# Optimization experiments

Measured on AMD Instinct MI355X. Metric: run time of the kernel, lower is better.

The kernel has to match this reference:

```python
import jax, jax.numpy as jnp
import numpy as np

NUM_GRAPHS = 512
N_NODES = 500000
C = 256
R = 16

def setup_inputs() -> dict:
    key = jax.random.key(0)
    k1, k2, k3, k4 = jax.random.split(key, 4)
    x = jax.random.normal(k1, (N_NODES, C), dtype=jnp.float32)
    batch = jnp.sort(jax.random.randint(k2, (N_NODES,), 0, NUM_GRAPHS, dtype=jnp.int64))
    # Linear weights (torch stores [out,in]; we use [in,out] for x @ W)
    W1 = jax.random.normal(k3, (C, C // R), dtype=jnp.float32) * (1.0 / np.sqrt(C))
    W2 = jax.random.normal(k4, (C // R, C), dtype=jnp.float32) * (1.0 / np.sqrt(C // R))
    return {"x": x, "batch": batch, "W1": W1, "W2": W2}

def reference(x, batch, W1, W2):
    batch = batch.astype(jnp.int32)
    # segment mean pool: [G, C]
    seg_sum = jax.ops.segment_sum(x, batch, num_segments=NUM_GRAPHS)
    counts = jax.ops.segment_sum(jnp.ones((x.shape[0],), x.dtype), batch, num_segments=NUM_GRAPHS)
    mean_pool = seg_sum / jnp.maximum(counts, 1.0)[:, None]
    # squeeze-excite MLP: Linear -> ReLU -> Linear -> Sigmoid
    scale = jax.nn.sigmoid(jax.nn.relu(mean_pool @ W1) @ W2)  # [G, C]
    # repeat_interleave(scale, bincount(batch)) on sorted batch == gather by batch
    return x * scale[batch]
```

## Files before the change

### kernel.cpp

```cpp
#include <hip/hip_runtime.h>

#define NCH 256
#define HID 16
#define NBLK 256

typedef __attribute__((ext_vector_type(4))) float f32x4;

__device__ __forceinline__ f32x4 ldrow(const float* __restrict__ x, int r, size_t coff) {
    return __builtin_nontemporal_load(reinterpret_cast<const f32x4*>(x + (size_t)r * NCH + coff));
}

__device__ __forceinline__ void strow(float* __restrict__ out, int r, size_t coff, f32x4 v) {
    __builtin_nontemporal_store(v, reinterpret_cast<f32x4*>(out + (size_t)r * NCH + coff));
}

__device__ __forceinline__ void se_mlp(const float* __restrict__ W1,
                                       const float* __restrict__ W2,
                                       float (&s_part)[16][NCH],
                                       int first, int npart, int cnt,
                                       float* __restrict__ s_vec,
                                       float (&s_hp)[HID][17], float (&s_h)[HID],
                                       int tid)
{
    if (tid < NCH) {
        float m = 0.f;
        for (int i = 0; i < npart; ++i) m += s_part[first + i][tid];
        m *= (cnt > 0) ? (1.0f / (float)cnt) : 1.0f;
        s_vec[tid] = m;
    }
    __syncthreads();
    if (tid < NCH) {
        const int j = tid >> 4, sub = tid & 15;
        float hp = 0.f;
        #pragma unroll
        for (int i = 0; i < 16; ++i) { int c = sub * 16 + i; hp += s_vec[c] * W1[c * HID + j]; }
        s_hp[j][sub] = hp;
    }
    __syncthreads();
    if (tid < HID) {
        float h = 0.f;
        #pragma unroll
        for (int i = 0; i < 16; ++i) h += s_hp[tid][i];
        s_h[tid] = fmaxf(h, 0.f);
    }
    __syncthreads();
    if (tid < NCH) {
        float sc = 0.f;
        #pragma unroll
        for (int j = 0; j < HID; ++j) sc += s_h[j] * W2[j * NCH + tid];
        s_vec[tid] = 1.0f / (1.0f + __expf(-sc));
    }
}

__global__ __launch_bounds__(1024, 4) void graph_se_kernel(
    const float* __restrict__ x,
    const int* __restrict__ batch,
    const float* __restrict__ W1,
    const float* __restrict__ W2,
    float* __restrict__ out,
    int n)
{
    const int b   = blockIdx.x;
    const int tid = threadIdx.x;

    __shared__ int   s_bnd[4];
    __shared__ float s_part[16][NCH];
    __shared__ float s_vecA[NCH];
    __shared__ float s_vecB[NCH];
    __shared__ float s_hp[HID][17];
    __shared__ float s_h[HID];

    if (tid < 4) {
        int v = (tid < 2) ? (b + tid) : (NBLK + b + (tid - 2));
        int lo = 0, hi = n;
        while (lo < hi) { int mid = (lo + hi) >> 1; if (batch[mid] < v) lo = mid + 1; else hi = mid; }
        s_bnd[tid] = lo;
    }
    __syncthreads();
    const int loA = s_bnd[0], hiA = s_bnd[1];
    const int loB = s_bnd[2], hiB = s_bnd[3];

    const int rg = tid >> 6;
    const int c4 = tid & 63;
    const size_t coff = (size_t)c4 * 4;

    {
        f32x4 acc = (f32x4)(0.f);
        int r = loA + rg;
        for (; r + 112 < hiA; r += 128) {
            f32x4 v0 = ldrow(x, r      , coff);
            f32x4 v1 = ldrow(x, r +  16, coff);
            f32x4 v2 = ldrow(x, r +  32, coff);
            f32x4 v3 = ldrow(x, r +  48, coff);
            f32x4 v4 = ldrow(x, r +  64, coff);
            f32x4 v5 = ldrow(x, r +  80, coff);
            f32x4 v6 = ldrow(x, r +  96, coff);
            f32x4 v7 = ldrow(x, r + 112, coff);
            acc += ((v0 + v1) + (v2 + v3)) + ((v4 + v5) + (v6 + v7));
        }
        for (; r < hiA; r += 16) acc += ldrow(x, r, coff);
        *reinterpret_cast<f32x4*>(&s_part[rg][c4 * 4]) = acc;
    }
    __syncthreads();

    se_mlp(W1, W2, s_part, 0, 16, hiA - loA, s_vecA, s_hp, s_h, tid);
    __syncthreads();

    if (rg < 8) {
        const f32x4 scv = *reinterpret_cast<const f32x4*>(&s_vecA[c4 * 4]);
        int r = loA + rg;
        for (; r + 24 < hiA; r += 32) {
            f32x4 v0 = ldrow(x, r     , coff);
            f32x4 v1 = ldrow(x, r +  8, coff);
            f32x4 v2 = ldrow(x, r + 16, coff);
            f32x4 v3 = ldrow(x, r + 24, coff);
            strow(out, r     , coff, v0 * scv);
            strow(out, r +  8, coff, v1 * scv);
            strow(out, r + 16, coff, v2 * scv);
            strow(out, r + 24, coff, v3 * scv);
        }
        for (; r < hiA; r += 8) {
            strow(out, r, coff, ldrow(x, r, coff) * scv);
        }
    } else {
        const int gid = rg - 8;
        f32x4 acc = (f32x4)(0.f);
        int r = loB + gid;
        for (; r + 56 < hiB; r += 64) {
            f32x4 v0 = ldrow(x, r     , coff);
            f32x4 v1 = ldrow(x, r +  8, coff);
            f32x4 v2 = ldrow(x, r + 16, coff);
            f32x4 v3 = ldrow(x, r + 24, coff);
            f32x4 v4 = ldrow(x, r + 32, coff);
            f32x4 v5 = ldrow(x, r + 40, coff);
            f32x4 v6 = ldrow(x, r + 48, coff);
            f32x4 v7 = ldrow(x, r + 56, coff);
            acc += ((v0 + v1) + (v2 + v3)) + ((v4 + v5) + (v6 + v7));
        }
        for (; r < hiB; r += 8) acc += ldrow(x, r, coff);
        *reinterpret_cast<f32x4*>(&s_part[rg][c4 * 4]) = acc;
    }
    __syncthreads();

    se_mlp(W1, W2, s_part, 8, 8, hiB - loB, s_vecB, s_hp, s_h, tid);
    __syncthreads();

    {
        const f32x4 scv = *reinterpret_cast<const f32x4*>(&s_vecB[c4 * 4]);
        int r = loB + rg;
        for (; r + 48 < hiB; r += 64) {
            f32x4 v0 = ldrow(x, r     , coff);
            f32x4 v1 = ldrow(x, r + 16, coff);
            f32x4 v2 = ldrow(x, r + 32, coff);
            f32x4 v3 = ldrow(x, r + 48, coff);
            strow(out, r     , coff, v0 * scv);
            strow(out, r + 16, coff, v1 * scv);
            strow(out, r + 32, coff, v2 * scv);
            strow(out, r + 48, coff, v3 * scv);
        }
        for (; r < hiB; r += 16) {
            strow(out, r, coff, ldrow(x, r, coff) * scv);
        }
    }
}

extern "C" void kernel_launch(void* const* d_in, const int* in_sizes, int n_in,
                              void* d_out, int out_size, void* d_ws, size_t ws_size,
                              hipStream_t stream) {
    const float* x     = (const float*)d_in[0];
    const int*   batch = (const int*)d_in[1];
    const float* W1    = (const float*)d_in[2];
    const float* W2    = (const float*)d_in[3];
    float*       out   = (float*)d_out;
    const int n = in_sizes[1];

    hipLaunchKernelGGL(graph_se_kernel, dim3(NBLK), dim3(1024), 0, stream,
                       x, batch, W1, W2, out, n);
}
```

Before: 285.0 us.

## Stash leading segment rows in registers and LDS to avoid re-reading x

Keeps the first 256 rows of segment A in per-thread registers and the next 128 rows in a 128 KB LDS stash during the pooling pass, then writes them scaled without re-reading global memory. For segment B, the first 128 rows are held in registers by the second half of the threads. Loads from x switch from nontemporal to regular so that rows read twice may hit in cache. The cost is far higher register and LDS use per block, which cuts occupancy, and segments average about 1000 rows, so only part of the re-read is removed.

```diff
diff --git a/kernel.cpp b/kernel.cpp
--- a/kernel.cpp
+++ b/kernel.cpp
@@ -3,11 +3,13 @@
 #define NCH 256
 #define HID 16
 #define NBLK 256
+#define SREG 16
+#define ALDS 128
 
 typedef __attribute__((ext_vector_type(4))) float f32x4;
 
 __device__ __forceinline__ f32x4 ldrow(const float* __restrict__ x, int r, size_t coff) {
-    return __builtin_nontemporal_load(reinterpret_cast<const f32x4*>(x + (size_t)r * NCH + coff));
+    return *reinterpret_cast<const f32x4*>(x + (size_t)r * NCH + coff);
 }
 
 __device__ __forceinline__ void strow(float* __restrict__ out, int r, size_t coff, f32x4 v) {
@@ -63,6 +65,7 @@
     const int b   = blockIdx.x;
     const int tid = threadIdx.x;
 
+    __shared__ float s_stash[ALDS][NCH];
     __shared__ int   s_bnd[4];
     __shared__ float s_part[16][NCH];
     __shared__ float s_vecA[NCH];
@@ -84,19 +87,32 @@
     const int c4 = tid & 63;
     const size_t coff = (size_t)c4 * 4;
 
+    f32x4 st[SREG];
+
     {
         f32x4 acc = (f32x4)(0.f);
-        int r = loA + rg;
-        for (; r + 112 < hiA; r += 128) {
-            f32x4 v0 = ldrow(x, r      , coff);
-            f32x4 v1 = ldrow(x, r +  16, coff);
-            f32x4 v2 = ldrow(x, r +  32, coff);
-            f32x4 v3 = ldrow(x, r +  48, coff);
-            f32x4 v4 = ldrow(x, r +  64, coff);
-            f32x4 v5 = ldrow(x, r +  80, coff);
-            f32x4 v6 = ldrow(x, r +  96, coff);
-            f32x4 v7 = ldrow(x, r + 112, coff);
-            acc += ((v0 + v1) + (v2 + v3)) + ((v4 + v5) + (v6 + v7));
+        const int base = loA + rg;
+        #pragma unroll
+        for (int k = 0; k < SREG; ++k) {
+            int rr = base + 16 * k;
+            if (rr < hiA) { st[k] = ldrow(x, rr, coff); acc += st[k]; }
+        }
+        #pragma unroll
+        for (int k = 0; k < 8; ++k) {
+            int rr = base + 16 * (SREG + k);
+            if (rr < hiA) {
+                f32x4 v = ldrow(x, rr, coff);
+                *reinterpret_cast<f32x4*>(&s_stash[rg + 16 * k][c4 * 4]) = v;
+                acc += v;
+            }
+        }
+        int r = loA + (16 * SREG + ALDS) + rg;
+        for (; r + 48 < hiA; r += 64) {
+            f32x4 v0 = ldrow(x, r     , coff);
+            f32x4 v1 = ldrow(x, r + 16, coff);
+            f32x4 v2 = ldrow(x, r + 32, coff);
+            f32x4 v3 = ldrow(x, r + 48, coff);
+            acc += (v0 + v1) + (v2 + v3);
         }
         for (; r < hiA; r += 16) acc += ldrow(x, r, coff);
         *reinterpret_cast<f32x4*>(&s_part[rg][c4 * 4]) = acc;
@@ -106,39 +122,55 @@
     se_mlp(W1, W2, s_part, 0, 16, hiA - loA, s_vecA, s_hp, s_h, tid);
     __syncthreads();
 
-    if (rg < 8) {
-        const f32x4 scv = *reinterpret_cast<const f32x4*>(&s_vecA[c4 * 4]);
-        int r = loA + rg;
-        for (; r + 24 < hiA; r += 32) {
-            f32x4 v0 = ldrow(x, r     , coff);
-            f32x4 v1 = ldrow(x, r +  8, coff);
-            f32x4 v2 = ldrow(x, r + 16, coff);
-            f32x4 v3 = ldrow(x, r + 24, coff);
-            strow(out, r     , coff, v0 * scv);
-            strow(out, r +  8, coff, v1 * scv);
-            strow(out, r + 16, coff, v2 * scv);
-            strow(out, r + 24, coff, v3 * scv);
-        }
-        for (; r < hiA; r += 8) {
-            strow(out, r, coff, ldrow(x, r, coff) * scv);
-        }
-    } else {
-        const int gid = rg - 8;
-        f32x4 acc = (f32x4)(0.f);
-        int r = loB + gid;
-        for (; r + 56 < hiB; r += 64) {
-            f32x4 v0 = ldrow(x, r     , coff);
-            f32x4 v1 = ldrow(x, r +  8, coff);
-            f32x4 v2 = ldrow(x, r + 16, coff);
-            f32x4 v3 = ldrow(x, r + 24, coff);
-            f32x4 v4 = ldrow(x, r + 32, coff);
-            f32x4 v5 = ldrow(x, r + 40, coff);
-            f32x4 v6 = ldrow(x, r + 48, coff);
-            f32x4 v7 = ldrow(x, r + 56, coff);
-            acc += ((v0 + v1) + (v2 + v3)) + ((v4 + v5) + (v6 + v7));
-        }
-        for (; r < hiB; r += 8) acc += ldrow(x, r, coff);
-        *reinterpret_cast<f32x4*>(&s_part[rg][c4 * 4]) = acc;
+    {
+        const f32x4 scvA = *reinterpret_cast<const f32x4*>(&s_vecA[c4 * 4]);
+        #pragma unroll
+        for (int k = 0; k < SREG; ++k) {
+            int rr = loA + rg + 16 * k;
+            if (rr < hiA) strow(out, rr, coff, st[k] * scvA);
+        }
+        if (rg < 8) {
+            #pragma unroll
+            for (int j = 0; j < 16; ++j) {
+                int i = rg + 8 * j;
+                int rr = loA + 16 * SREG + i;
+                if (rr < hiA) {
+                    f32x4 v = *reinterpret_cast<const f32x4*>(&s_stash[i][c4 * 4]);
+                    strow(out, rr, coff, v * scvA);
+                }
+            }
+            int r = loA + (16 * SREG + ALDS) + rg;
+            for (; r + 24 < hiA; r += 32) {
+                f32x4 v0 = ldrow(x, r     , coff);
+                f32x4 v1 = ldrow(x, r +  8, coff);
+                f32x4 v2 = ldrow(x, r + 16, coff);
+                f32x4 v3 = ldrow(x, r + 24, coff);
+                strow(out, r     , coff, v0 * scvA);
+                strow(out, r +  8, coff, v1 * scvA);
+                strow(out, r + 16, coff, v2 * scvA);
+                strow(out, r + 24, coff, v3 * scvA);
+            }
+            for (; r < hiA; r += 8) strow(out, r, coff, ldrow(x, r, coff) * scvA);
+        } else {
+            const int gid = rg - 8;
+            f32x4 acc = (f32x4)(0.f);
+            const int baseB = loB + gid;
+            #pragma unroll
+            for (int k = 0; k < SREG; ++k) {
+                int rr = baseB + 8 * k;
+                if (rr < hiB) { st[k] = ldrow(x, rr, coff); acc += st[k]; }
+            }
+            int r = baseB + 8 * SREG;
+            for (; r + 24 < hiB; r += 32) {
+                f32x4 v0 = ldrow(x, r     , coff);
+                f32x4 v1 = ldrow(x, r +  8, coff);
+                f32x4 v2 = ldrow(x, r + 16, coff);
+                f32x4 v3 = ldrow(x, r + 24, coff);
+                acc += (v0 + v1) + (v2 + v3);
+            }
+            for (; r < hiB; r += 8) acc += ldrow(x, r, coff);
+            *reinterpret_cast<f32x4*>(&s_part[rg][c4 * 4]) = acc;
+        }
     }
     __syncthreads();
 
@@ -146,21 +178,27 @@
     __syncthreads();
 
     {
-        const f32x4 scv = *reinterpret_cast<const f32x4*>(&s_vecB[c4 * 4]);
-        int r = loB + rg;
+        const f32x4 scvB = *reinterpret_cast<const f32x4*>(&s_vecB[c4 * 4]);
+        if (rg >= 8) {
+            const int gid = rg - 8;
+            #pragma unroll
+            for (int k = 0; k < SREG; ++k) {
+                int rr = loB + gid + 8 * k;
+                if (rr < hiB) strow(out, rr, coff, st[k] * scvB);
+            }
+        }
+        int r = loB + 8 * SREG + rg;
         for (; r + 48 < hiB; r += 64) {
             f32x4 v0 = ldrow(x, r     , coff);
             f32x4 v1 = ldrow(x, r + 16, coff);
             f32x4 v2 = ldrow(x, r + 32, coff);
             f32x4 v3 = ldrow(x, r + 48, coff);
-            strow(out, r     , coff, v0 * scv);
-            strow(out, r + 16, coff, v1 * scv);
-            strow(out, r + 32, coff, v2 * scv);
-            strow(out, r + 48, coff, v3 * scv);
-        }
-        for (; r < hiB; r += 16) {
-            strow(out, r, coff, ldrow(x, r, coff) * scv);
-        }
+            strow(out, r     , coff, v0 * scvB);
+            strow(out, r + 16, coff, v1 * scvB);
+            strow(out, r + 32, coff, v2 * scvB);
+            strow(out, r + 48, coff, v3 * scvB);
+        }
+        for (; r < hiB; r += 16) strow(out, r, coff, ldrow(x, r, coff) * scvB);
     }
 }
 
```

Measured after the change: 252.3 us. -11.5%, faster.
